# Performance work log

Hardware: AMD Instinct MI355X
Metric: run time of the kernel (lower is better)

Reference implementation:

```python
import jax, jax.numpy as jnp
import numpy as np
import math

B, S, D, H = 4, 2048, 1024, 16
DK = D // H  # 64


def setup_inputs() -> dict:
    key = jax.random.key(0)
    ks = jax.random.split(key, 10)
    scale = 1.0 / math.sqrt(D)
    inp = {
        "context_sequence": jax.random.normal(ks[0], (B, S, D), dtype=jnp.float32),
        "value_sequence": jax.random.normal(ks[1], (B, S, D), dtype=jnp.float32),
        "mask": jax.random.randint(ks[2], (S, S), 0, 2, dtype=jnp.int32),
        # stacked per-head projection params: [H, D, DK] weights, [H, DK] biases
        "Wq": jax.random.uniform(ks[3], (H, D, DK), jnp.float32, -scale, scale),
        "bq": jnp.zeros((H, DK), jnp.float32),
        "Wk": jax.random.uniform(ks[4], (H, D, DK), jnp.float32, -scale, scale),
        "bk": jnp.zeros((H, DK), jnp.float32),
        "Wv": jax.random.uniform(ks[5], (H, D, DK), jnp.float32, -scale, scale),
        "bv": jnp.zeros((H, DK), jnp.float32),
        "Wo": jax.random.uniform(ks[6], (D, D), jnp.float32, -scale, scale),
        "bo": jnp.zeros((D,), jnp.float32),
    }
    return inp


def reference(context_sequence, value_sequence, mask, Wq, bq, Wk, bk, Wv, bv, Wo, bo):
    # per-head projections batched over heads: [B,H,S,DK]
    Q = jnp.einsum("bsd,hdk->bhsk", context_sequence, Wq) + bq[None, :, None, :]
    K = jnp.einsum("bsd,hdk->bhsk", context_sequence, Wk) + bk[None, :, None, :]
    V = jnp.einsum("bsd,hdk->bhsk", value_sequence, Wv) + bv[None, :, None, :]
    scores = jnp.einsum("bhsk,bhtk->bhst", Q, K) / math.sqrt(DK)
    scores = jnp.where(mask[None, None, :, :] == 1, jnp.float32(-1e9), scores)
    attn = jax.nn.softmax(scores, axis=-1)
    out = jnp.einsum("bhst,bhtk->bhsk", attn, V)  # [B,H,S,DK]
    concat = out.transpose(0, 2, 1, 3).reshape(B, S, D)  # heads concatenated
    # output projection (dropout is identity in eval mode)
    return concat @ Wo.T + bo
```

## Files before the change

### kernel.cpp

```cpp
#include <hip/hip_runtime.h>
#include <hip/hip_bf16.h>

#define DEVI __device__ __forceinline__

typedef __attribute__((ext_vector_type(8))) short bf16x8;
typedef __attribute__((ext_vector_type(4))) float f32x4;
typedef unsigned short u16;
typedef unsigned long long u64;


DEVI void async16(const void* g, const void* l) {
  __builtin_amdgcn_global_load_lds(
      (const __attribute__((address_space(1))) unsigned int*)g,
      (__attribute__((address_space(3))) unsigned int*)l, 16, 0, 0);
}

DEVI u16 f2bf(float x) {
  unsigned int u = __float_as_uint(x);
  return (u16)((u + 0x7fffu + ((u >> 16) & 1u)) >> 16);
}

DEVI float fast_exp2(float x) {
#if __has_builtin(__builtin_amdgcn_exp2f)
  return __builtin_amdgcn_exp2f(x);
#else
  return exp2f(x);
#endif
}

DEVI unsigned pk_bf16(unsigned hi, unsigned lo) {
#if __has_builtin(__builtin_amdgcn_perm)
  return __builtin_amdgcn_perm(hi, lo, 0x07060302u);
#else
  return (hi & 0xffff0000u) | (lo >> 16);
#endif
}


__global__ __launch_bounds__(256) void prep_kernel(
    const float* __restrict__ ctx, const float* __restrict__ val, const int* __restrict__ msk,
    const float* __restrict__ Wq, const float* __restrict__ Wk, const float* __restrict__ Wv,
    const float* __restrict__ Wo, const float* __restrict__ bq, const float* __restrict__ bk,
    u16* __restrict__ Xc, u16* __restrict__ Xv, u16* __restrict__ Wqt, u16* __restrict__ Wkt,
    u16* __restrict__ Wvt, u16* __restrict__ WoB, u64* __restrict__ mbits, float* __restrict__ bqk) {
  __shared__ float tile[64 * 69];
  const int blk = blockIdx.x, tid = threadIdx.x;
  if (blk < 16384) {
    const float* src = (blk < 8192) ? ctx : val;
    u16* dst = (blk < 8192) ? Xc : Xv;
    int i = (blk & 8191) * 256 + tid;
    float4 v = ((const float4*)src)[i];
    ushort4 o;
    o.x = f2bf(v.x); o.y = f2bf(v.y); o.z = f2bf(v.z); o.w = f2bf(v.w);
    ((ushort4*)dst)[i] = o;
  } else if (blk < 17408) {
    int i = (blk - 16384) * 256 + tid;
    float4 v = ((const float4*)Wo)[i];
    ushort4 o;
    o.x = f2bf(v.x); o.y = f2bf(v.y); o.z = f2bf(v.z); o.w = f2bf(v.w);
    ((ushort4*)WoB)[i] = o;
  } else if (blk < 18176) {
    int t = blk - 17408;
    int mat = t >> 8, r = t & 255, h = r >> 4, d0 = (r & 15) * 64;
    const float* Ws = (mat == 0) ? Wq : (mat == 1) ? Wk : Wv;
    u16* Wd = (mat == 0) ? Wqt : (mat == 1) ? Wkt : Wvt;
    const int dg = tid & 15, rg = tid >> 4;
#pragma unroll
    for (int i = 0; i < 4; i++) {
      int dr = rg + i * 16;
      float4 v = *(const float4*)&Ws[((size_t)(h * 1024 + d0 + dr)) * 64 + dg * 4];
      tile[dr * 69 + dg * 4 + 0] = v.x;
      tile[dr * 69 + dg * 4 + 1] = v.y;
      tile[dr * 69 + dg * 4 + 2] = v.z;
      tile[dr * 69 + dg * 4 + 3] = v.w;
    }
    __syncthreads();
#pragma unroll
    for (int i = 0; i < 4; i++) {
      int k = rg + i * 16;
      ushort4 o;
      o.x = f2bf(tile[(dg * 4 + 0) * 69 + k]);
      o.y = f2bf(tile[(dg * 4 + 1) * 69 + k]);
      o.z = f2bf(tile[(dg * 4 + 2) * 69 + k]);
      o.w = f2bf(tile[(dg * 4 + 3) * 69 + k]);
      *(ushort4*)&Wd[(size_t)(h * 64 + k) * 1024 + d0 + dg * 4] = o;
    }
  } else if (blk < 34560) {
    int gid = (blk - 18176) * 256 + tid;
    u64 bal = __ballot(msk[gid] == 1);
    if ((tid & 63) == 0) mbits[(size_t)((gid >> 6) & 31) * 2048 + (gid >> 11)] = bal;
  } else {
    int i = (blk - 34560) * 256 + tid;
    bqk[i] = (i < 1024) ? bq[i] : bk[i - 1024];
  }
}


__global__ __launch_bounds__(256) void qkv_gemm(const u16* __restrict__ Xc, const u16* __restrict__ Xv,
                                                const u16* __restrict__ Wqkt, const u16* __restrict__ Wvt,
                                                const float* __restrict__ bqk, const float* __restrict__ bvv,
                                                u16* __restrict__ QKb, u16* __restrict__ Vtg, float qscale) {
  __shared__ __align__(16) u16 As[128 * 32];
  __shared__ __align__(16) u16 Bs[128 * 32];
  const int tid = threadIdx.x;
  const int w = tid >> 6, lane = tid & 63, quad = lane >> 4, lc = lane & 15;
  const int K = 1024;
  const bool isV = blockIdx.y >= 16;
  const int m0 = blockIdx.x * 128;
  const int n0 = (isV ? (blockIdx.y - 16) : blockIdx.y) * 128;
  const u16* A  = isV ? Xv : Xc;
  const u16* Bt = isV ? Wvt : Wqkt;
  const float* bias = isV ? bvv : bqk;
  const int wrow = (w >> 1) * 64, wcol = (w & 1) * 64;
  const int srow = tid >> 2, sc = tid & 3;
  const u16* Ag = A + (size_t)(m0 + srow) * K + sc * 8;
  const u16* Bg = Bt + (size_t)(n0 + srow) * K + sc * 8;
  u16* Asw = As + w * 512;
  u16* Bsw = Bs + w * 512;

  f32x4 acc[4][4] = {};
  for (int k0 = 0; k0 < K; k0 += 32) {
    async16(Ag + k0, Asw);
    async16(Ag + k0 + (size_t)64 * K, Asw + 2048);
    async16(Bg + k0, Bsw);
    async16(Bg + k0 + (size_t)64 * K, Bsw + 2048);
    __syncthreads();
    bf16x8 af[4], bfr[4];
#pragma unroll
    for (int rt = 0; rt < 4; rt++) af[rt] = *(const bf16x8*)&As[(wrow + rt * 16 + lc) * 32 + quad * 8];
#pragma unroll
    for (int ct = 0; ct < 4; ct++) bfr[ct] = *(const bf16x8*)&Bs[(wcol + ct * 16 + lc) * 32 + quad * 8];
#pragma unroll
    for (int rt = 0; rt < 4; rt++)
#pragma unroll
      for (int ct = 0; ct < 4; ct++)
        acc[rt][ct] = __builtin_amdgcn_mfma_f32_16x16x32_bf16(af[rt], bfr[ct], acc[rt][ct], 0, 0, 0);
    __syncthreads();
  }
#pragma unroll
  for (int ct = 0; ct < 4; ct++) {
    int col = n0 + wcol + ct * 16 + lc;
    float bv = bias[col];
    float os = (!isV && col < 1024) ? qscale : 1.0f;
#pragma unroll
    for (int rt = 0; rt < 4; rt++) {
      if (isV) {
        int trow = m0 + wrow + rt * 16 + quad * 4;
        ushort4 pk;
        pk.x = f2bf(acc[rt][ct][0] + bv);
        pk.y = f2bf(acc[rt][ct][1] + bv);
        pk.z = f2bf(acc[rt][ct][2] + bv);
        pk.w = f2bf(acc[rt][ct][3] + bv);
        size_t off = ((size_t)(trow >> 11) * 1024 + col) * 2048 + (trow & 2047);
        *(ushort4*)(Vtg + off) = pk;
      } else {
#pragma unroll
        for (int r = 0; r < 4; r++) {
          int row = m0 + wrow + rt * 16 + quad * 4 + r;
          QKb[(size_t)row * 2048 + col] = f2bf((acc[rt][ct][r] + bv) * os);
        }
      }
    }
  }
}


__global__ __launch_bounds__(256, 4) void attn_kernel(const u16* __restrict__ QK, const u16* __restrict__ Vt,
                                                      const u64* __restrict__ mbits, u16* __restrict__ AO) {
  __shared__ __align__(16) u16 Ks[2][4096];
  __shared__ __align__(16) u16 Vs[2][4096];
  const int S = 2048, D = 1024, QS = 2048;
  const int tid = threadIdx.x, w = tid >> 6, lane = tid & 63, quad = lane >> 4, lc = lane & 15;
  const int q0 = blockIdx.x * 128;
  const int b = blockIdx.y >> 4, h = blockIdx.y & 15;
  const size_t baseq = (size_t)b * S * QS + (size_t)h * 64;
  const size_t vbase = (size_t)blockIdx.y * 64 * S;
  const int sr = lane >> 3, gch = (lane & 7) ^ sr, lx = lc & 7;
  u16* Ksq = (u16*)Ks;

#pragma unroll
  for (int i = 0; i < 4; i++) {
    const u16* g = QK + baseq + (size_t)(q0 + w * 32 + i * 8 + sr) * QS + gch * 8;
    async16(g, Ksq + w * 2048 + i * 512);
  }
  const int kperm = 32 * (w & 1) + 4 * (w >> 1) + 8 * (sr >> 2) + (sr & 3);
  const u16* Kg0 = QK + baseq + 1024 + (size_t)kperm * QS + gch * 8;
  const u16* Vg0 = Vt + vbase + (size_t)(w * 16 + sr) * S + gch * 8;
  __syncthreads();

  bf16x8 aq[2][2];
#pragma unroll
  for (int s = 0; s < 2; s++)
#pragma unroll
    for (int ks = 0; ks < 2; ks++)
      aq[s][ks] = *(const bf16x8*)&Ksq[w * 2048 + (s * 16 + lc) * 64 + (((ks * 4 + quad) ^ lx) << 3)];
  __syncthreads();

  async16(Kg0, Ks[0] + w * 1024);
  async16(Kg0 + (size_t)16 * QS, Ks[0] + w * 1024 + 512);
  async16(Vg0, Vs[0] + w * 1024);
  async16(Vg0 + (size_t)8 * S, Vs[0] + w * 1024 + 512);

  const u64* mptr = mbits + (size_t)(q0 + w * 32 + lc);

  bf16x8 ones;
#pragma unroll
  for (int j = 0; j < 8; j++) ones[j] = (short)0x3F80;

  f32x4 acco[2][4] = {};
  f32x4 accl[2] = {};

  for (int t0 = 0; t0 < S; t0 += 64) {
    const int cur = (t0 >> 6) & 1;
    __syncthreads();
    if (t0 + 64 < S) {
      const u16* Kg = Kg0 + (size_t)(t0 + 64) * QS;
      const u16* Vg = Vg0 + (t0 + 64);
      async16(Kg, Ks[cur ^ 1] + w * 1024);
      async16(Kg + (size_t)16 * QS, Ks[cur ^ 1] + w * 1024 + 512);
      async16(Vg, Vs[cur ^ 1] + w * 1024);
      async16(Vg + (size_t)8 * S, Vs[cur ^ 1] + w * 1024 + 512);
    }

    u64 mw0 = mptr[(size_t)(t0 >> 6) * 2048];
    u64 mw1 = mptr[(size_t)(t0 >> 6) * 2048 + 16];

    f32x4 sacc[2][4] = {};
    __builtin_amdgcn_s_setprio(1);
#pragma unroll
    for (int ks = 0; ks < 2; ks++)
#pragma unroll
      for (int ct = 0; ct < 4; ct++) {
        bf16x8 bk = *(const bf16x8*)&Ks[cur][(ct * 16 + lc) * 64 + (((ks * 4 + quad) ^ lx) << 3)];
        sacc[0][ct] = __builtin_amdgcn_mfma_f32_16x16x32_bf16(bk, aq[0][ks], sacc[0][ct], 0, 0, 0);
        sacc[1][ct] = __builtin_amdgcn_mfma_f32_16x16x32_bf16(bk, aq[1][ks], sacc[1][ct], 0, 0, 0);
      }
    __builtin_amdgcn_s_setprio(0);

#pragma unroll
    for (int s = 0; s < 2; s++) {
      u64 wq = (s == 0 ? mw0 : mw1) >> (quad * 8);
      unsigned lo = (unsigned)wq, hi = (unsigned)(wq >> 32);
      unsigned pu[4][4];
#pragma unroll
      for (int ct = 0; ct < 4; ct++) {
        unsigned bits = (ct & 1) ? hi : lo;
        const int sh = (ct >> 1) * 4;
#pragma unroll
        for (int r = 0; r < 4; r++)
          pu[ct][r] = __float_as_uint(fast_exp2(((bits >> (sh + r)) & 1u) ? -1e4f : sacc[s][ct][r]));
      }
      union { unsigned u[4]; bf16x8 v; } f0, f1;
      f0.u[0] = pk_bf16(pu[0][1], pu[0][0]);
      f0.u[1] = pk_bf16(pu[0][3], pu[0][2]);
      f0.u[2] = pk_bf16(pu[2][1], pu[2][0]);
      f0.u[3] = pk_bf16(pu[2][3], pu[2][2]);
      f1.u[0] = pk_bf16(pu[1][1], pu[1][0]);
      f1.u[1] = pk_bf16(pu[1][3], pu[1][2]);
      f1.u[2] = pk_bf16(pu[3][1], pu[3][0]);
      f1.u[3] = pk_bf16(pu[3][3], pu[3][2]);

      __builtin_amdgcn_s_setprio(1);
#pragma unroll
      for (int ct = 0; ct < 4; ct++) {
        bf16x8 bv = *(const bf16x8*)&Vs[cur][(ct * 16 + lc) * 64 + ((quad ^ lx) << 3)];
        acco[s][ct] = __builtin_amdgcn_mfma_f32_16x16x32_bf16(f0.v, bv, acco[s][ct], 0, 0, 0);
      }
      accl[s] = __builtin_amdgcn_mfma_f32_16x16x32_bf16(f0.v, ones, accl[s], 0, 0, 0);
#pragma unroll
      for (int ct = 0; ct < 4; ct++) {
        bf16x8 bv = *(const bf16x8*)&Vs[cur][(ct * 16 + lc) * 64 + (((4 + quad) ^ lx) << 3)];
        acco[s][ct] = __builtin_amdgcn_mfma_f32_16x16x32_bf16(f1.v, bv, acco[s][ct], 0, 0, 0);
      }
      accl[s] = __builtin_amdgcn_mfma_f32_16x16x32_bf16(f1.v, ones, accl[s], 0, 0, 0);
      __builtin_amdgcn_s_setprio(0);
    }
  }

#pragma unroll
  for (int s = 0; s < 2; s++)
#pragma unroll
    for (int r = 0; r < 4; r++) {
      float inv = 1.0f / accl[s][r];
      size_t row = (size_t)b * S + q0 + w * 32 + s * 16 + quad * 4 + r;
#pragma unroll
      for (int ct = 0; ct < 4; ct++)
        AO[row * D + h * 64 + ct * 16 + lc] = f2bf(acco[s][ct][r] * inv);
    }
}


__global__ __launch_bounds__(256) void out_gemm(const u16* __restrict__ A, const u16* __restrict__ Bt,
                                                const float* __restrict__ bias, float* __restrict__ C) {
  __shared__ __align__(16) u16 As[128 * 32];
  __shared__ __align__(16) u16 Bs[128 * 32];
  const int tid = threadIdx.x;
  const int w = tid >> 6, lane = tid & 63, quad = lane >> 4, lc = lane & 15;
  const int K = 1024, N = 1024;
  const int m0 = blockIdx.x * 128, n0 = blockIdx.y * 128;
  const int wrow = (w >> 1) * 64, wcol = (w & 1) * 64;
  const int srow = tid >> 2, sc = tid & 3;
  const u16* Ag = A + (size_t)(m0 + srow) * K + sc * 8;
  const u16* Bg = Bt + (size_t)(n0 + srow) * K + sc * 8;
  u16* Asw = As + w * 512;
  u16* Bsw = Bs + w * 512;

  f32x4 acc[4][4] = {};
  for (int k0 = 0; k0 < K; k0 += 32) {
    async16(Ag + k0, Asw);
    async16(Ag + k0 + (size_t)64 * K, Asw + 2048);
    async16(Bg + k0, Bsw);
    async16(Bg + k0 + (size_t)64 * K, Bsw + 2048);
    __syncthreads();
    bf16x8 af[4], bfr[4];
#pragma unroll
    for (int rt = 0; rt < 4; rt++) af[rt] = *(const bf16x8*)&As[(wrow + rt * 16 + lc) * 32 + quad * 8];
#pragma unroll
    for (int ct = 0; ct < 4; ct++) bfr[ct] = *(const bf16x8*)&Bs[(wcol + ct * 16 + lc) * 32 + quad * 8];
#pragma unroll
    for (int rt = 0; rt < 4; rt++)
#pragma unroll
      for (int ct = 0; ct < 4; ct++)
        acc[rt][ct] = __builtin_amdgcn_mfma_f32_16x16x32_bf16(af[rt], bfr[ct], acc[rt][ct], 0, 0, 0);
    __syncthreads();
  }
#pragma unroll
  for (int ct = 0; ct < 4; ct++) {
    int col = n0 + wcol + ct * 16 + lc;
    float bv = bias[col];
#pragma unroll
    for (int rt = 0; rt < 4; rt++)
#pragma unroll
      for (int r = 0; r < 4; r++) {
        int row = m0 + wrow + rt * 16 + quad * 4 + r;
        C[(size_t)row * N + col] = acc[rt][ct][r] + bv;
      }
  }
}


extern "C" void kernel_launch(void* const* d_in, const int* in_sizes, int n_in,
                              void* d_out, int out_size, void* d_ws, size_t ws_size,
                              hipStream_t stream) {
  const int B = 4, S = 2048, D = 1024;
  const float* ctx = (const float*)d_in[0];
  const float* val = (const float*)d_in[1];
  const int*   msk = (const int*)d_in[2];
  const float* Wq  = (const float*)d_in[3];
  const float* bq  = (const float*)d_in[4];
  const float* Wk  = (const float*)d_in[5];
  const float* bk  = (const float*)d_in[6];
  const float* Wv  = (const float*)d_in[7];
  const float* bv  = (const float*)d_in[8];
  const float* Wo  = (const float*)d_in[9];
  const float* bo  = (const float*)d_in[10];
  float* out = (float*)d_out;

  char* ws = (char*)d_ws;
  size_t off = 0;
  auto alloc = [&](size_t sz) { void* p = ws + off; off += (sz + 255) & ~255ULL; return p; };
  const size_t NTOK = (size_t)B * S * D;
  u16* Xc  = (u16*)alloc(NTOK * 2);
  u16* Xv  = (u16*)alloc(NTOK * 2);
  u16* Wqt = (u16*)alloc((size_t)D * D * 2);
  u16* Wkt = (u16*)alloc((size_t)D * D * 2);
  u16* Wvt = (u16*)alloc((size_t)D * D * 2);
  u16* WoB = (u16*)alloc((size_t)D * D * 2);
  u16* QKb = (u16*)alloc(NTOK * 4);
  u16* Vtg = (u16*)alloc(NTOK * 2);
  u64* mbits = (u64*)alloc((size_t)S * S / 8);
  float* bqk = (float*)alloc(2048 * 4);
  u16* AO = Xc;
  if (off > ws_size) return;

  const float qscale = 0.125f * 1.44269504088896f;

  prep_kernel<<<34568, 256, 0, stream>>>(ctx, val, msk, Wq, Wk, Wv, Wo, bq, bk,
                                         Xc, Xv, Wqt, Wkt, Wvt, WoB, mbits, bqk);

  qkv_gemm<<<dim3(B * S / 128, 24), 256, 0, stream>>>(Xc, Xv, Wqt, Wvt, bqk, bv, QKb, Vtg, qscale);

  attn_kernel<<<dim3(S / 128, B * 16), 256, 0, stream>>>(QKb, Vtg, mbits, AO);

  out_gemm<<<dim3(B * S / 128, D / 128), 256, 0, stream>>>(AO, WoB, bo, out);
}
```

Baseline: 340.9 us.

## Replace mask bitfield with bf16 AND-mask stored in output buffer

The mask is now pre-expanded into a 16-bit per-element AND-mask (0 or 0xFFFF), staged in the output buffer, instead of a packed 64-bit ballot bitfield. The attention loop applies it by ANDing the packed bf16 probabilities rather than doing per-element bit extraction and selects before exp2. The score MFMAs also start from a zero constant instead of zero-initialised accumulators, and the main loop is unrolled by two. The aim is fewer VALU instructions in the softmax path, at the cost of 16x more mask traffic (8 MB versus 0.5 MB read per batch-head sweep) and reliance on reusing the output buffer as scratch.

```diff
diff --git a/kernel.cpp b/kernel.cpp
--- a/kernel.cpp
+++ b/kernel.cpp
@@ -42,7 +42,7 @@
     const float* __restrict__ Wq, const float* __restrict__ Wk, const float* __restrict__ Wv,
     const float* __restrict__ Wo, const float* __restrict__ bq, const float* __restrict__ bk,
     u16* __restrict__ Xc, u16* __restrict__ Xv, u16* __restrict__ Wqt, u16* __restrict__ Wkt,
-    u16* __restrict__ Wvt, u16* __restrict__ WoB, u64* __restrict__ mbits, float* __restrict__ bqk) {
+    u16* __restrict__ Wvt, u16* __restrict__ WoB, u16* __restrict__ Mm, float* __restrict__ bqk) {
   __shared__ float tile[64 * 69];
   const int blk = blockIdx.x, tid = threadIdx.x;
   if (blk < 16384) {
@@ -85,12 +85,17 @@
       o.w = f2bf(tile[(dg * 4 + 3) * 69 + k]);
       *(ushort4*)&Wd[(size_t)(h * 64 + k) * 1024 + d0 + dg * 4] = o;
     }
-  } else if (blk < 34560) {
-    int gid = (blk - 18176) * 256 + tid;
-    u64 bal = __ballot(msk[gid] == 1);
-    if ((tid & 63) == 0) mbits[(size_t)((gid >> 6) & 31) * 2048 + (gid >> 11)] = bal;
+  } else if (blk < 22272) {
+    int i = (blk - 18176) * 256 + tid;
+    int4 m4 = ((const int4*)msk)[i];
+    ushort4 o;
+    o.x = (m4.x == 1) ? (u16)0 : (u16)0xFFFFu;
+    o.y = (m4.y == 1) ? (u16)0 : (u16)0xFFFFu;
+    o.z = (m4.z == 1) ? (u16)0 : (u16)0xFFFFu;
+    o.w = (m4.w == 1) ? (u16)0 : (u16)0xFFFFu;
+    ((ushort4*)Mm)[i] = o;
   } else {
-    int i = (blk - 34560) * 256 + tid;
+    int i = (blk - 22272) * 256 + tid;
     bqk[i] = (i < 1024) ? bq[i] : bk[i - 1024];
   }
 }
@@ -166,7 +171,7 @@
 
 
 __global__ __launch_bounds__(256, 4) void attn_kernel(const u16* __restrict__ QK, const u16* __restrict__ Vt,
-                                                      const u64* __restrict__ mbits, u16* __restrict__ AO) {
+                                                      const u16* __restrict__ Mm, u16* __restrict__ AO) {
   __shared__ __align__(16) u16 Ks[2][4096];
   __shared__ __align__(16) u16 Vs[2][4096];
   const int S = 2048, D = 1024, QS = 2048;
@@ -201,15 +206,18 @@
   async16(Vg0, Vs[0] + w * 1024);
   async16(Vg0 + (size_t)8 * S, Vs[0] + w * 1024 + 512);
 
-  const u64* mptr = mbits + (size_t)(q0 + w * 32 + lc);
+  const u16* Mr0 = Mm + (size_t)(q0 + w * 32 + lc) * 2048 + quad * 8;
+  const u16* Mr1 = Mr0 + (size_t)16 * 2048;
 
   bf16x8 ones;
 #pragma unroll
   for (int j = 0; j < 8; j++) ones[j] = (short)0x3F80;
 
+  const f32x4 z = {};
   f32x4 acco[2][4] = {};
   f32x4 accl[2] = {};
 
+#pragma unroll 2
   for (int t0 = 0; t0 < S; t0 += 64) {
     const int cur = (t0 >> 6) & 1;
     __syncthreads();
@@ -222,43 +230,46 @@
       async16(Vg + (size_t)8 * S, Vs[cur ^ 1] + w * 1024 + 512);
     }
 
-    u64 mw0 = mptr[(size_t)(t0 >> 6) * 2048];
-    u64 mw1 = mptr[(size_t)(t0 >> 6) * 2048 + 16];
-
-    f32x4 sacc[2][4] = {};
+    uint4 ma0 = *(const uint4*)(Mr0 + t0);
+    uint4 mb0 = *(const uint4*)(Mr0 + t0 + 32);
+    uint4 ma1 = *(const uint4*)(Mr1 + t0);
+    uint4 mb1 = *(const uint4*)(Mr1 + t0 + 32);
+
+    f32x4 sacc[2][4];
     __builtin_amdgcn_s_setprio(1);
 #pragma unroll
-    for (int ks = 0; ks < 2; ks++)
-#pragma unroll
-      for (int ct = 0; ct < 4; ct++) {
-        bf16x8 bk = *(const bf16x8*)&Ks[cur][(ct * 16 + lc) * 64 + (((ks * 4 + quad) ^ lx) << 3)];
-        sacc[0][ct] = __builtin_amdgcn_mfma_f32_16x16x32_bf16(bk, aq[0][ks], sacc[0][ct], 0, 0, 0);
-        sacc[1][ct] = __builtin_amdgcn_mfma_f32_16x16x32_bf16(bk, aq[1][ks], sacc[1][ct], 0, 0, 0);
-      }
+    for (int ct = 0; ct < 4; ct++) {
+      bf16x8 bk = *(const bf16x8*)&Ks[cur][(ct * 16 + lc) * 64 + ((quad ^ lx) << 3)];
+      sacc[0][ct] = __builtin_amdgcn_mfma_f32_16x16x32_bf16(bk, aq[0][0], z, 0, 0, 0);
+      sacc[1][ct] = __builtin_amdgcn_mfma_f32_16x16x32_bf16(bk, aq[1][0], z, 0, 0, 0);
+    }
+#pragma unroll
+    for (int ct = 0; ct < 4; ct++) {
+      bf16x8 bk = *(const bf16x8*)&Ks[cur][(ct * 16 + lc) * 64 + (((4 + quad) ^ lx) << 3)];
+      sacc[0][ct] = __builtin_amdgcn_mfma_f32_16x16x32_bf16(bk, aq[0][1], sacc[0][ct], 0, 0, 0);
+      sacc[1][ct] = __builtin_amdgcn_mfma_f32_16x16x32_bf16(bk, aq[1][1], sacc[1][ct], 0, 0, 0);
+    }
     __builtin_amdgcn_s_setprio(0);
 
 #pragma unroll
     for (int s = 0; s < 2; s++) {
-      u64 wq = (s == 0 ? mw0 : mw1) >> (quad * 8);
-      unsigned lo = (unsigned)wq, hi = (unsigned)(wq >> 32);
+      const uint4 mA = s ? ma1 : ma0;
+      const uint4 mB = s ? mb1 : mb0;
       unsigned pu[4][4];
 #pragma unroll
-      for (int ct = 0; ct < 4; ct++) {
-        unsigned bits = (ct & 1) ? hi : lo;
-        const int sh = (ct >> 1) * 4;
+      for (int ct = 0; ct < 4; ct++)
 #pragma unroll
         for (int r = 0; r < 4; r++)
-          pu[ct][r] = __float_as_uint(fast_exp2(((bits >> (sh + r)) & 1u) ? -1e4f : sacc[s][ct][r]));
-      }
+          pu[ct][r] = __float_as_uint(fast_exp2(sacc[s][ct][r]));
       union { unsigned u[4]; bf16x8 v; } f0, f1;
-      f0.u[0] = pk_bf16(pu[0][1], pu[0][0]);
-      f0.u[1] = pk_bf16(pu[0][3], pu[0][2]);
-      f0.u[2] = pk_bf16(pu[2][1], pu[2][0]);
-      f0.u[3] = pk_bf16(pu[2][3], pu[2][2]);
-      f1.u[0] = pk_bf16(pu[1][1], pu[1][0]);
-      f1.u[1] = pk_bf16(pu[1][3], pu[1][2]);
-      f1.u[2] = pk_bf16(pu[3][1], pu[3][0]);
-      f1.u[3] = pk_bf16(pu[3][3], pu[3][2]);
+      f0.u[0] = pk_bf16(pu[0][1], pu[0][0]) & mA.x;
+      f0.u[1] = pk_bf16(pu[0][3], pu[0][2]) & mA.y;
+      f0.u[2] = pk_bf16(pu[2][1], pu[2][0]) & mA.z;
+      f0.u[3] = pk_bf16(pu[2][3], pu[2][2]) & mA.w;
+      f1.u[0] = pk_bf16(pu[1][1], pu[1][0]) & mB.x;
+      f1.u[1] = pk_bf16(pu[1][3], pu[1][2]) & mB.y;
+      f1.u[2] = pk_bf16(pu[3][1], pu[3][0]) & mB.z;
+      f1.u[3] = pk_bf16(pu[3][3], pu[3][2]) & mB.w;
 
       __builtin_amdgcn_s_setprio(1);
 #pragma unroll
@@ -368,19 +379,19 @@
   u16* WoB = (u16*)alloc((size_t)D * D * 2);
   u16* QKb = (u16*)alloc(NTOK * 4);
   u16* Vtg = (u16*)alloc(NTOK * 2);
-  u64* mbits = (u64*)alloc((size_t)S * S / 8);
   float* bqk = (float*)alloc(2048 * 4);
   u16* AO = Xc;
+  u16* Mm = (u16*)out;
   if (off > ws_size) return;
 
   const float qscale = 0.125f * 1.44269504088896f;
 
-  prep_kernel<<<34568, 256, 0, stream>>>(ctx, val, msk, Wq, Wk, Wv, Wo, bq, bk,
-                                         Xc, Xv, Wqt, Wkt, Wvt, WoB, mbits, bqk);
+  prep_kernel<<<22280, 256, 0, stream>>>(ctx, val, msk, Wq, Wk, Wv, Wo, bq, bk,
+                                         Xc, Xv, Wqt, Wkt, Wvt, WoB, Mm, bqk);
 
   qkv_gemm<<<dim3(B * S / 128, 24), 256, 0, stream>>>(Xc, Xv, Wqt, Wvt, bqk, bv, QKb, Vtg, qscale);
 
-  attn_kernel<<<dim3(S / 128, B * 16), 256, 0, stream>>>(QKb, Vtg, mbits, AO);
+  attn_kernel<<<dim3(S / 128, B * 16), 256, 0, stream>>>(QKb, Vtg, Mm, AO);
 
   out_gemm<<<dim3(B * S / 128, D / 128), 256, 0, stream>>>(AO, WoB, bo, out);
 }
```

Measured after the change: 419.0 us. 22.9% more time.
